# Kernel optimization log

Hardware: AMD Instinct MI355X
Metric: run time of the kernel (lower is better)

## Reference

```python
import jax, jax.numpy as jnp
import numpy as np

NUM_HEADS = 8
H_DIM = 24
COORDS_DIM = 3
NUM_W_PER_DIST = 8
BLOCK_SIZE = 128
N_HASHES = 3
N = 32768
HASH_DIM = H_DIM + (COORDS_DIM - 1) + 2  # q/k augmented with RPE coordinate terms


def layernorm(x, g, b, eps=1e-5):
    mu = x.mean(-1, keepdims=True)
    var = ((x - mu) ** 2).mean(-1, keepdims=True)
    return (x - mu) * jax.lax.rsqrt(var + eps) * g + b


def setup_inputs() -> dict:
    key = jax.random.key(0)
    ks = jax.random.split(key, 16)
    d, H = H_DIM, NUM_HEADS
    s = lambda i, shape, scale: jax.random.normal(ks[i], shape, jnp.float32) * scale
    return {
        "x": s(0, (N, d), 1.0),
        "coords": jax.random.uniform(ks[1], (N, COORDS_DIM), jnp.float32),
        "norm1_g": jnp.ones((d,), jnp.float32),
        "norm1_b": jnp.zeros((d,), jnp.float32),
        "Wq": s(2, (d, H * d), d ** -0.5),
        "Wk": s(3, (d, H * d), d ** -0.5),
        "Wv": s(4, (d, H * d), d ** -0.5),
        "w_rpe_W": s(5, (H * d, (COORDS_DIM - 1) * NUM_W_PER_DIST), 0.3),
        "Wo": s(6, (H * d, d), (H * d) ** -0.5),
        "bo": jnp.zeros((d,), jnp.float32),
        "norm2_g": jnp.ones((d,), jnp.float32),
        "norm2_b": jnp.zeros((d,), jnp.float32),
        "ff_W1": s(7, (d, d), d ** -0.5),
        "ff_b1": jnp.zeros((d,), jnp.float32),
        "ff_W2": s(8, (d, d), d ** -0.5),
        "ff_b2": jnp.zeros((d,), jnp.float32),
        "alphas": s(9, (N_HASHES, H, HASH_DIM), 1.0),  # E2LSH projection vectors
    }


def hept_attention(q, k, v, coords, w_rpe_W, alphas):
    # q,k,v: [n, H*d]. HEPT: fold RPE exp(-w*||dp||^2) into augmented q/k, then
    # n_hashes rounds of LSH sort + block-local attention, combined by softmax
    # over each round's log-normalizer (Reformer-style).
    n = q.shape[0]
    H, d, B = NUM_HEADS, H_DIM, BLOCK_SIZE
    nb = n // B
    q = q.reshape(n, H, d).transpose(1, 0, 2) * (d ** -0.5)  # [H,n,d]
    k = k.reshape(n, H, d).transpose(1, 0, 2)
    v = v.reshape(n, H, d).transpose(1, 0, 2)
    # per-head non-negative distance weights from w_rpe (mixture collapsed)
    Wm = w_rpe_W.reshape(H, d, COORDS_DIM - 1, NUM_W_PER_DIST)
    w = jnp.mean(Wm, axis=(1, 3)) ** 2                        # [H, c-1]
    p = coords[:, 1:]                                          # [n, c-1]
    sqn = jnp.einsum("hc,nc,nc->hn", w, p, p)                # w*||p||^2
    qp = jnp.sqrt(2.0) * jnp.sqrt(w)[:, None, :] * p[None]     # [H,n,c-1]
    ones = jnp.ones((H, n, 1), q.dtype)
    # q_hat.k_hat = q.k + 2*w*p_i.p_j - w|p_i|^2 - w|p_j|^2 = q.k - w*||p_i-p_j||^2
    q_hat = jnp.concatenate([q, qp, -sqn[..., None], ones], -1)  # [H,n,HASH_DIM]
    k_hat = jnp.concatenate([k, qp, ones, -sqn[..., None]], -1)
    outs, zs = [], []
    for r in range(N_HASHES):
        a = alphas[r]                                          # [H, HASH_DIM]
        iq = jnp.argsort(jnp.einsum("hne,he->hn", q_hat, a), -1)
        ik = jnp.argsort(jnp.einsum("hne,he->hn", k_hat, a), -1)
        qs = jnp.take_along_axis(q_hat, iq[..., None], 1).reshape(H, nb, B, -1)
        ks = jnp.take_along_axis(k_hat, ik[..., None], 1).reshape(H, nb, B, -1)
        vs = jnp.take_along_axis(v, ik[..., None], 1).reshape(H, nb, B, d)
        logits = jnp.einsum("hbqe,hbke->hbqk", qs, ks)         # [H,nb,B,B]
        z = jax.nn.logsumexp(logits, -1).reshape(H, n)
        o = jnp.einsum("hbqk,hbkd->hbqd", jax.nn.softmax(logits, -1), vs).reshape(H, n, d)
        inv = jnp.argsort(iq, -1)                              # unsort to input order
        outs.append(jnp.take_along_axis(o, inv[..., None], 1))
        zs.append(jnp.take_along_axis(z, inv, 1))
    wts = jax.nn.softmax(jnp.stack(zs), axis=0)[..., None]     # [R,H,n,1]
    out = (jnp.stack(outs) * wts).sum(0)                       # [H,n,d]
    return out.transpose(1, 0, 2).reshape(n, H * d)


def reference(x, coords, norm1_g, norm1_b, Wq, Wk, Wv, w_rpe_W, Wo, bo,
              norm2_g, norm2_b, ff_W1, ff_b1, ff_W2, ff_b2, alphas):
    xn = layernorm(x, norm1_g, norm1_b)
    q, k, v = xn @ Wq, xn @ Wk, xn @ Wv
    aggr = hept_attention(q, k, v, coords, w_rpe_W, alphas) @ Wo + bo
    x = x + aggr  # dropout is identity in eval mode
    h = layernorm(x, norm2_g, norm2_b)
    ff = jax.nn.relu(h @ ff_W1 + ff_b1) @ ff_W2 + ff_b2
    return x + ff
```

## Files before the change

kernel.cpp:

```cpp
#include <hip/hip_runtime.h>
#include <math.h>

#define NPT 32768
#define NH 8
#define HD 24
#define EDIM 28
#define NHASH 3
#define NSEG 48
#define NRH 24

typedef unsigned long long u64;
typedef unsigned short ushort;
typedef __attribute__((__vector_size__(8 * sizeof(short)))) short bf16x8;
typedef __attribute__((__vector_size__(4 * sizeof(float)))) float floatx4;
typedef __attribute__((__vector_size__(4 * sizeof(unsigned int)))) unsigned int uint32x4;

__device__ __forceinline__ ushort f2bf(float f) {
    unsigned u = __float_as_uint(f);
    unsigned r = u + 0x7FFF + ((u >> 16) & 1);
    return (ushort)(r >> 16);
}
__device__ __forceinline__ float us2f(ushort u) {
    return __uint_as_float(((unsigned)u) << 16);
}

__global__ __launch_bounds__(256) void k0b(
    const float* __restrict__ wrpe, const float* __restrict__ Wq,
    const float* __restrict__ Wk, const float* __restrict__ alphas,
    double* __restrict__ w64, double* __restrict__ cqp64,
    double* __restrict__ Aq, double* __restrict__ Ak, double* __restrict__ ct) {
    __shared__ double sw[16], sc[16];
    int t = threadIdx.x;
    if (t < 16) {
        int h = t >> 1, c = t & 1;
        double s = 0.0;
        for (int i = 0; i < 24; i++)
            for (int j = 0; j < 8; j++)
                s += (double)wrpe[(h * 24 + i) * 16 + c * 8 + j];
        double m = s / 192.0;
        sw[t] = m * m;
        sc[t] = sqrt(2.0) * fabs(m);
        w64[t] = sw[t];
        cqp64[t] = sc[t];
    }
    __syncthreads();
    const double QSCALE = 1.0 / sqrt(24.0);
    for (int idx = t; idx < 24 * NRH; idx += 256) {
        int i = idx / NRH, rh = idx % NRH;
        int h = rh & 7;
        double aq = 0.0, ak = 0.0;
        for (int e = 0; e < 24; e++) {
            double al = (double)alphas[rh * 28 + e];
            aq += (double)Wq[i * 192 + h * 24 + e] * al;
            ak += (double)Wk[i * 192 + h * 24 + e] * al;
        }
        Aq[idx] = aq * QSCALE;
        Ak[idx] = ak;
    }
    if (t < NRH) {
        int h = t & 7;
        ct[t * 4 + 0] = (double)alphas[t * 28 + 24] * sc[h * 2 + 0];
        ct[t * 4 + 1] = (double)alphas[t * 28 + 25] * sc[h * 2 + 1];
        ct[t * 4 + 2] = (double)alphas[t * 28 + 26];
        ct[t * 4 + 3] = (double)alphas[t * 28 + 27];
    }
}

__global__ __launch_bounds__(512) void k2s(
    const float* __restrict__ x, const float* __restrict__ n1g,
    const float* __restrict__ n1b, const float* __restrict__ coords,
    const double* __restrict__ Aq, const double* __restrict__ Ak,
    const double* __restrict__ ct, const double* __restrict__ w64,
    u64* __restrict__ keys, float* __restrict__ xnf) {
    __shared__ double sA[2][24][NRH];
    __shared__ double sCt[NRH][4];
    __shared__ double sW64[16];
    __shared__ double sGB[48];
    __shared__ double sXn[8][24];
    int t = threadIdx.x;
    for (int i = t; i < 24 * NRH; i += 512) sA[0][i / NRH][i % NRH] = Aq[i];
    for (int i = t; i < 24 * NRH; i += 512) sA[1][i / NRH][i % NRH] = Ak[i];
    for (int i = t; i < NRH * 4; i += 512) sCt[i / 4][i % 4] = ct[i];
    if (t < 16) sW64[t] = w64[t];
    if (t < 24) { sGB[t] = (double)n1g[t]; sGB[24 + t] = (double)n1b[t]; }
    __syncthreads();
    int wv = t >> 6, l = t & 63;
    for (int g = 0; g < 8; g++) {
        int n = blockIdx.x * 64 + g * 8 + wv;
        double xv = (l < 24) ? (double)x[(u64)n * 24 + l] : 0.0;
        double s = xv;
        s += __shfl_xor(s, 1); s += __shfl_xor(s, 2); s += __shfl_xor(s, 4);
        s += __shfl_xor(s, 8); s += __shfl_xor(s, 16);
        double mu = s / 24.0;
        double d = (l < 24) ? (xv - mu) : 0.0;
        double v2 = d * d;
        v2 += __shfl_xor(v2, 1); v2 += __shfl_xor(v2, 2); v2 += __shfl_xor(v2, 4);
        v2 += __shfl_xor(v2, 8); v2 += __shfl_xor(v2, 16);
        double rstd = 1.0 / sqrt(v2 / 24.0 + 1e-5);
        if (l < 24) {
            double xn = d * rstd * sGB[l] + sGB[24 + l];
            sXn[wv][l] = xn;
            xnf[(u64)n * 24 + l] = (float)xn;
        }
        double p0 = (double)coords[(u64)n * 3 + 1];
        double p1 = (double)coords[(u64)n * 3 + 2];
        if (l < 2 * NRH) {
            int qk = l / NRH, rh = l % NRH;
            int h = rh & 7;
            double sqn = sW64[2 * h] * p0 * p0 + sW64[2 * h + 1] * p1 * p1;
            double acc = sCt[rh][0] * p0 + sCt[rh][1] * p1;
            acc += qk ? (sCt[rh][2] - sqn * sCt[rh][3]) : (sCt[rh][3] - sqn * sCt[rh][2]);
            for (int i = 0; i < 24; i++) acc += sXn[wv][i] * sA[qk][i][rh];
            u64 u = (u64)__double_as_longlong(acc);
            if (u >> 63) u = ~u; else u |= 0x8000000000000000ULL;
            u64 key = (u & ~(u64)32767) | (u64)n;
            keys[(u64)l * NPT + n] = key;
        }
    }
}

#define K2P_PTS 32
__global__ __launch_bounds__(640) void k2p(
    const float* __restrict__ xnf,
    const float* __restrict__ Wq, const float* __restrict__ Wk,
    const float* __restrict__ Wv, const float* __restrict__ coords,
    const double* __restrict__ w64, const double* __restrict__ cqp64,
    ushort* __restrict__ qhatB, ushort* __restrict__ khatB, ushort* __restrict__ varrB) {
    __shared__ __align__(16) ushort sT[3 * 8 * K2P_PTS * 32];
    int t = threadIdx.x;
    int n0 = blockIdx.x * K2P_PTS;
    if (t < 576) {
        int m = t / 192, jj = t % 192;
        const float* W = (m == 0) ? Wq : ((m == 1) ? Wk : Wv);
        float wc[24];
#pragma unroll
        for (int i = 0; i < 24; i++) wc[i] = W[i * 192 + jj];
        const float scale = (m == 0) ? (float)(1.0 / sqrt(24.0)) : 1.0f;
        int h = jj / 24, e = jj % 24;
        ushort* sbase = sT + ((m * 8 + h) * K2P_PTS) * 32 + e;
        for (int p = 0; p < K2P_PTS; p++) {
            int n = n0 + p;
            const float* xr = xnf + (u64)n * 24;
            float acc = 0.f;
#pragma unroll
            for (int i = 0; i < 24; i++) acc += xr[i] * wc[i];
            sbase[p * 32] = f2bf(acc * scale);
        }
    } else {
        int l = t - 576;
        int h2 = l >> 3, e2 = 24 + (l & 7);
        double c0 = cqp64[h2 * 2], c1 = cqp64[h2 * 2 + 1];
        double wa = w64[h2 * 2], wb = w64[h2 * 2 + 1];
        ushort* qb = sT + ((0 * 8 + h2) * K2P_PTS) * 32 + e2;
        ushort* kb = sT + ((1 * 8 + h2) * K2P_PTS) * 32 + e2;
        ushort* vb = sT + ((2 * 8 + h2) * K2P_PTS) * 32 + e2;
        for (int p = 0; p < K2P_PTS; p++) {
            int n = n0 + p;
            double p0 = (double)coords[(u64)n * 3 + 1];
            double p1 = (double)coords[(u64)n * 3 + 2];
            float qv, kv;
            if (e2 < 26) {
                int c = e2 - 24;
                float qp = (float)((c ? c1 : c0) * (c ? p1 : p0));
                qv = qp; kv = qp;
            } else if (e2 < 28) {
                double sqn = wa * p0 * p0 + wb * p1 * p1;
                if (e2 == 26) { qv = (float)(-sqn); kv = 1.0f; }
                else          { qv = 1.0f; kv = (float)(-sqn); }
            } else {
                qv = 0.0f; kv = 0.0f;
            }
            qb[p * 32] = f2bf(qv);
            kb[p * 32] = f2bf(kv);
            vb[p * 32] = 0;
        }
    }
    __syncthreads();
    for (int c = t; c < 3 * 8 * K2P_PTS * 4; c += 640) {
        int arrh = c >> 7, off = c & 127;
        int arr = arrh >> 3, hh = arrh & 7;
        uint32x4 v = *(const uint32x4*)(sT + arrh * (K2P_PTS * 32) + off * 8);
        ushort* op = (arr == 0) ? qhatB : ((arr == 1) ? khatB : varrB);
        *(uint32x4*)(op + (u64)hh * NPT * 32 + (u64)n0 * 32 + off * 8) = v;
    }
}

__device__ __forceinline__ u64 shflx64(u64 v, int d) {
    int lo = __shfl_xor((int)(unsigned)v, d);
    int hi = __shfl_xor((int)(unsigned)(v >> 32), d);
    return ((u64)(unsigned)hi << 32) | (unsigned)lo;
}
__device__ __forceinline__ void cswap(u64& a, u64& b, bool up) {
    if ((a > b) == up) { u64 tmp = a; a = b; b = tmp; }
}
__device__ __forceinline__ u64* sslot(u64* s, int i) {
    int a = i << 3;
    a ^= ((a >> 9) & 7) << 4;
    return (u64*)((char*)s + a);
}
__device__ __forceinline__ void reg_passes(u64 e[8], int ib, int K, int jmax) {
    for (int j = jmax; j >= 1; j >>= 1) {
#pragma unroll
        for (int k = 0; k < 8; k++)
            if ((k & j) == 0) cswap(e[k], e[k | j], ((ib + k) & K) == 0);
    }
}
__device__ __forceinline__ void shfl_passes(u64 e[8], int t, int segoff, int K, int jhi, int jlo) {
    for (int j = jhi; j >= jlo; j >>= 1) {
        int d = j >> 3;
        bool lower = (t & d) == 0;
        bool up = ((segoff + ((t & ~d) << 3)) & K) == 0;
        bool keepmin = (lower == up);
#pragma unroll
        for (int k = 0; k < 8; k++) {
            u64 o = shflx64(e[k], d);
            bool ownsm = e[k] < o;
            e[k] = (ownsm == keepmin) ? e[k] : o;
        }
    }
}

__global__ __launch_bounds__(1024) void sort_local_full(u64* keys) {
    __shared__ u64 s[8192];
    int t = threadIdx.x;
    u64 gbase = (u64)blockIdx.x * 8192;
    int segoff = (int)(gbase & 32767);
    int ib = segoff + t * 8;
    u64 e[8];
#pragma unroll
    for (int k = 0; k < 8; k++) e[k] = keys[gbase + t * 8 + k];
    reg_passes(e, ib, 2, 1);
    reg_passes(e, ib, 4, 2);
    reg_passes(e, ib, 8, 4);
    for (int K = 16; K <= 512; K <<= 1) {
        shfl_passes(e, t, segoff, K, K >> 1, 8);
        reg_passes(e, ib, K, 4);
    }
#pragma unroll
    for (int k = 0; k < 8; k++) *sslot(s, t * 8 + k) = e[k];
    __syncthreads();
    for (int K = 1024; K <= 8192; K <<= 1) {
        for (int j = K >> 1; j >= 512; j >>= 1) {
            for (int p = t; p < 4096; p += 1024) {
                int i = ((p & ~(j - 1)) << 1) | (p & (j - 1));
                int i2 = i | j;
                bool up = (((segoff + i) & K) == 0);
                u64 a = *sslot(s, i), b = *sslot(s, i2);
                if ((a > b) == up) { *sslot(s, i) = b; *sslot(s, i2) = a; }
            }
            __syncthreads();
        }
#pragma unroll
        for (int k = 0; k < 8; k++) e[k] = *sslot(s, t * 8 + k);
        shfl_passes(e, t, segoff, K, 256, 8);
        reg_passes(e, ib, K, 4);
        if (K < 8192) {
#pragma unroll
            for (int k = 0; k < 8; k++) *sslot(s, t * 8 + k) = e[k];
            __syncthreads();
        } else {
#pragma unroll
            for (int k = 0; k < 8; k++) keys[gbase + t * 8 + k] = e[k];
        }
    }
}

__global__ __launch_bounds__(1024) void sort_tail1_fused(u64* keys) {
    __shared__ u64 s[8192];
    int t = threadIdx.x;
    u64 gbase = (u64)blockIdx.x * 8192;
    u64 pbase = gbase ^ 8192ULL;
    int ci = (int)((gbase >> 13) & 3);
    bool keepmin = (ci == 0) || (ci == 3);
    int segoff = (int)(gbase & 32767);
    int ib = segoff + t * 8;
    for (int i = t; i < 8192; i += 1024) {
        u64 a = keys[gbase + i];
        u64 b = keys[pbase + i];
        u64 mn = a < b ? a : b;
        u64 mx = a < b ? b : a;
        *sslot(s, i) = keepmin ? mn : mx;
    }
    __syncthreads();
    const int K = 16384;
    for (int j = 4096; j >= 512; j >>= 1) {
        for (int p = t; p < 4096; p += 1024) {
            int i = ((p & ~(j - 1)) << 1) | (p & (j - 1));
            int i2 = i | j;
            bool up = (((segoff + i) & K) == 0);
            u64 a = *sslot(s, i), b = *sslot(s, i2);
            if ((a > b) == up) { *sslot(s, i) = b; *sslot(s, i2) = a; }
        }
        __syncthreads();
    }
    u64 e[8];
#pragma unroll
    for (int k = 0; k < 8; k++) e[k] = *sslot(s, t * 8 + k);
    shfl_passes(e, t, segoff, K, 256, 8);
    reg_passes(e, ib, K, 4);
#pragma unroll
    for (int k = 0; k < 8; k++) keys[gbase + t * 8 + k] = e[k];
}

__global__ __launch_bounds__(1024) void sort_local_tail(u64* keys, int K, int minj) {
    __shared__ u64 s[8192];
    int t = threadIdx.x;
    u64 gbase = (u64)blockIdx.x * 8192;
    int segoff = (int)(gbase & 32767);
    int ib = segoff + t * 8;
    for (int i = t; i < 8192; i += 1024) *sslot(s, i) = keys[gbase + i];
    __syncthreads();
    for (int j = 4096; j >= 512; j >>= 1) {
        for (int p = t; p < 4096; p += 1024) {
            int i = ((p & ~(j - 1)) << 1) | (p & (j - 1));
            int i2 = i | j;
            bool up = (((segoff + i) & K) == 0);
            u64 a = *sslot(s, i), b = *sslot(s, i2);
            if ((a > b) == up) { *sslot(s, i) = b; *sslot(s, i2) = a; }
        }
        __syncthreads();
    }
    u64 e[8];
#pragma unroll
    for (int k = 0; k < 8; k++) e[k] = *sslot(s, t * 8 + k);
    shfl_passes(e, t, segoff, K, 256, minj >= 8 ? minj : 8);
    if (minj < 8) reg_passes(e, ib, K, 4);
#pragma unroll
    for (int k = 0; k < 8; k++) keys[gbase + t * 8 + k] = e[k];
}

__global__ void sort_global2(u64* keys) {
    int p = blockIdx.x * blockDim.x + threadIdx.x;
    if (p >= NSEG * 8192) return;
    int seg = p >> 13, c = p & 8191;
    u64 base = (u64)seg * 32768 + c;
    u64 e0 = keys[base];
    u64 e1 = keys[base + 8192];
    u64 e2 = keys[base + 16384];
    u64 e3 = keys[base + 24576];
    u64 tmp;
    if (e0 > e2) { tmp = e0; e0 = e2; e2 = tmp; }
    if (e1 > e3) { tmp = e1; e1 = e3; e3 = tmp; }
    if (e0 > e1) { tmp = e0; e0 = e1; e1 = tmp; }
    if (e2 > e3) { tmp = e2; e2 = e3; e3 = tmp; }
    keys[base] = e0;
    keys[base + 8192] = e1;
    keys[base + 16384] = e2;
    keys[base + 24576] = e3;
}

__global__ __launch_bounds__(256, 4) void k3_attn(
    const u64* __restrict__ keys, const ushort* __restrict__ qhatB,
    const ushort* __restrict__ khatB, const ushort* __restrict__ varrB,
    ushort* __restrict__ ozB) {
    int rh3 = blockIdx.x % 24;
    int b = blockIdx.x / 24;
    int h = rh3 & 7, r = rh3 >> 3;
    __shared__ __align__(16) char smem[6144 + 32768 + 512];
    char* sVt = smem;
    char* sP  = smem + 6144;
    ushort* qidx = (ushort*)(smem + 6144 + 32768);
    ushort* kidx = qidx + 128;
    int t = threadIdx.x;
    int segQ = r * 8 + h, segK = 24 + r * 8 + h;
    if (t < 128) {
        qidx[t] = (ushort)(keys[(u64)segQ * NPT + b * 128 + t] & 32767ULL);
    } else {
        int i = t - 128;
        kidx[i] = (ushort)(keys[(u64)segK * NPT + b * 128 + i] & 32767ULL);
    }
    __syncthreads();

    int wave = t >> 6, L = t & 63;
    int quad = L >> 4, n16 = L & 15;

    const bf16x8* Qg = (const bf16x8*)(qhatB + (u64)h * NPT * 32);
    const bf16x8* Kg = (const bf16x8*)(khatB + (u64)h * NPT * 32);
    bf16x8 afr[2];
#pragma unroll
    for (int rtg = 0; rtg < 2; rtg++) {
        int qi = qidx[wave * 32 + rtg * 16 + n16];
        afr[rtg] = Qg[(u64)qi * 4 + quad];
    }
    bf16x8 bfr[8];
#pragma unroll
    for (int ct = 0; ct < 8; ct++) {
        int ki = kidx[ct * 16 + n16];
        bfr[ct] = Kg[(u64)ki * 4 + quad];
    }
    if (t < 128) {
        int ki = kidx[t];
        const bf16x8* vr = (const bf16x8*)(varrB + ((u64)h * NPT + ki) * 32);
        bf16x8 v0 = vr[0], v1 = vr[1], v2 = vr[2];
        int colb = ((t & 15) << 4) | ((t >> 4) << 1);
#pragma unroll
        for (int e = 0; e < 8; e++) {
            int e0 = e, e1 = 8 + e, e2 = 16 + e;
            *(short*)(sVt + e0 * 256 + (colb ^ ((e0 & 7) << 4))) = v0[e];
            *(short*)(sVt + e1 * 256 + (colb ^ ((e1 & 7) << 4))) = v1[e];
            *(short*)(sVt + e2 * 256 + (colb ^ ((e2 & 7) << 4))) = v2[e];
        }
    }
    __syncthreads();

    floatx4 acc[2][8];
#pragma unroll
    for (int rtg = 0; rtg < 2; rtg++)
#pragma unroll
        for (int ct = 0; ct < 8; ct++)
            acc[rtg][ct] = (floatx4){0.f, 0.f, 0.f, 0.f};
#pragma unroll
    for (int ct = 0; ct < 8; ct++) {
#pragma unroll
        for (int rtg = 0; rtg < 2; rtg++)
            acc[rtg][ct] = __builtin_amdgcn_mfma_f32_16x16x32_bf16(afr[rtg], bfr[ct], acc[rtg][ct], 0, 0, 0);
    }

    float mrow[2][4], srow[2][4];
#pragma unroll
    for (int rtg = 0; rtg < 2; rtg++) {
#pragma unroll
        for (int rg = 0; rg < 4; rg++) {
            float m = acc[rtg][0][rg];
#pragma unroll
            for (int ct = 1; ct < 8; ct++) m = fmaxf(m, acc[rtg][ct][rg]);
            m = fmaxf(m, __shfl_xor(m, 1));
            m = fmaxf(m, __shfl_xor(m, 2));
            m = fmaxf(m, __shfl_xor(m, 4));
            m = fmaxf(m, __shfl_xor(m, 8));
            mrow[rtg][rg] = m;
            float p[8];
            float s = 0.0f;
#pragma unroll
            for (int ct = 0; ct < 8; ct++) {
                p[ct] = __expf(acc[rtg][ct][rg] - m);
                s += p[ct];
            }
            s += __shfl_xor(s, 1);
            s += __shfl_xor(s, 2);
            s += __shfl_xor(s, 4);
            s += __shfl_xor(s, 8);
            srow[rtg][rg] = s;
            unsigned w0, w1, w2, w3;
            asm("v_cvt_pk_bf16_f32 %0, %1, %2" : "=v"(w0) : "v"(p[0]), "v"(p[1]));
            asm("v_cvt_pk_bf16_f32 %0, %1, %2" : "=v"(w1) : "v"(p[2]), "v"(p[3]));
            asm("v_cvt_pk_bf16_f32 %0, %1, %2" : "=v"(w2) : "v"(p[4]), "v"(p[5]));
            asm("v_cvt_pk_bf16_f32 %0, %1, %2" : "=v"(w3) : "v"(p[6]), "v"(p[7]));
            int row = wave * 32 + rtg * 16 + quad * 4 + rg;
            uint32x4 pk = {w0, w1, w2, w3};
            *(uint32x4*)(sP + row * 256 + (((n16 << 4)) ^ ((row & 7) << 4))) = pk;
        }
    }

    floatx4 occ[2][2];
#pragma unroll
    for (int rtg = 0; rtg < 2; rtg++)
#pragma unroll
        for (int ct2 = 0; ct2 < 2; ct2++)
            occ[rtg][ct2] = (floatx4){0.f, 0.f, 0.f, 0.f};
#pragma unroll
    for (int ks = 0; ks < 4; ks++) {
        int kb = ks * 64 + quad * 16;
        bf16x8 bv[2], av[2];
#pragma unroll
        for (int ct2 = 0; ct2 < 2; ct2++) {
            int e = ct2 * 16 + n16;
            int ec = (e < 24) ? e : 0;
            bv[ct2] = *(const bf16x8*)(sVt + ec * 256 + (kb ^ ((ec & 7) << 4)));
        }
#pragma unroll
        for (int rtg = 0; rtg < 2; rtg++) {
            int rowA = wave * 32 + rtg * 16 + n16;
            av[rtg] = *(const bf16x8*)(sP + rowA * 256 + (kb ^ ((rowA & 7) << 4)));
        }
#pragma unroll
        for (int rtg = 0; rtg < 2; rtg++)
#pragma unroll
            for (int ct2 = 0; ct2 < 2; ct2++)
                occ[rtg][ct2] = __builtin_amdgcn_mfma_f32_16x16x32_bf16(av[rtg], bv[ct2], occ[rtg][ct2], 0, 0, 0);
    }

#pragma unroll
    for (int rtg = 0; rtg < 2; rtg++) {
#pragma unroll
        for (int rg = 0; rg < 4; rg++) {
            int row = wave * 32 + rtg * 16 + quad * 4 + rg;
            int oi = qidx[row];
            float inv = 1.0f / srow[rtg][rg];
            ushort* orow = ozB + ((u64)segQ * NPT + oi) * 32;
#pragma unroll
            for (int ct2 = 0; ct2 < 2; ct2++) {
                int col = ct2 * 16 + n16;
                if (col < 24) orow[col] = f2bf(occ[rtg][ct2][rg] * inv);
            }
            if (n16 == 0)
                *(float*)(orow + 24) = mrow[rtg][rg] + __logf(srow[rtg][rg]);
        }
    }
}

#define K4PTS 32
#define AT_STR 196
#define W_STR 28
__global__ __launch_bounds__(256) void k4_final(
    const ushort* __restrict__ ozB,
    const float* __restrict__ x,
    const float* __restrict__ Wo, const float* __restrict__ bo,
    const float* __restrict__ g2, const float* __restrict__ b2,
    const float* __restrict__ W1, const float* __restrict__ b1f,
    const float* __restrict__ W2, const float* __restrict__ b2f,
    float* __restrict__ out) {
    __shared__ __align__(16) float sWoT[24][AT_STR];
    __shared__ __align__(16) float sW1T[24][W_STR], sW2T[24][W_STR];
    __shared__ float sB[5 * 24];
    __shared__ __align__(16) float attn[K4PTS][AT_STR];
    __shared__ float xrow[K4PTS][25];
    __shared__ __align__(16) float h2row[K4PTS][W_STR];
    __shared__ __align__(16) float ffrow[K4PTS][W_STR];
    int t = threadIdx.x;
    int base = blockIdx.x * K4PTS;
    for (int i = t; i < 4608; i += 256) sWoT[i % 24][i / 24] = Wo[i];
    for (int i = t; i < 576; i += 256) {
        sW1T[i % 24][i / 24] = W1[i];
        sW2T[i % 24][i / 24] = W2[i];
    }
    if (t < 24) {
        sB[t] = bo[t]; sB[24 + t] = g2[t]; sB[48 + t] = b2[t];
        sB[72 + t] = b1f[t]; sB[96 + t] = b2f[t];
    }
    if (t < K4PTS * 4) {
        int p = t >> 2, c = 24 + (t & 3);
        h2row[p][c] = 0.f; ffrow[p][c] = 0.f;
    }
    if (t < 24 * 4) {
        int rr = t >> 2, c = 24 + (t & 3);
        sW1T[rr][c] = 0.f; sW2T[rr][c] = 0.f;
    }
    {
        int p = t >> 3, h = t & 7;
        int n = base + p;
        const ushort* r0 = ozB + ((u64)(0 * 8 + h) * NPT + n) * 32;
        const ushort* r1 = ozB + ((u64)(1 * 8 + h) * NPT + n) * 32;
        const ushort* r2 = ozB + ((u64)(2 * 8 + h) * NPT + n) * 32;
        float z0 = *(const float*)(r0 + 24);
        float z1 = *(const float*)(r1 + 24);
        float z2 = *(const float*)(r2 + 24);
        float zm = fmaxf(z0, fmaxf(z1, z2));
        float e0 = __expf(z0 - zm), e1 = __expf(z1 - zm), e2 = __expf(z2 - zm);
        float inv = 1.0f / (e0 + e1 + e2);
        float w0 = e0 * inv, w1 = e1 * inv, w2 = e2 * inv;
#pragma unroll
        for (int e = 0; e < 24; e++)
            attn[p][h * 24 + e] = w0 * us2f(r0[e]) + w1 * us2f(r1[e]) + w2 * us2f(r2[e]);
    }
    __syncthreads();
    int p = t >> 3, oe = t & 7;
    int n = base + p;
    {
        const floatx4* ap = (const floatx4*)&attn[p][0];
        const floatx4* w0p = (const floatx4*)&sWoT[oe][0];
        const floatx4* w1p = (const floatx4*)&sWoT[oe + 8][0];
        const floatx4* w2p = (const floatx4*)&sWoT[oe + 16][0];
        floatx4 A0 = {0.f, 0.f, 0.f, 0.f}, A1 = A0, A2 = A0;
        for (int ii = 0; ii < 48; ii++) {
            floatx4 av = ap[ii];
            A0 += av * w0p[ii];
            A1 += av * w1p[ii];
            A2 += av * w2p[ii];
        }
        float a0 = A0[0] + A0[1] + A0[2] + A0[3];
        float a1 = A1[0] + A1[1] + A1[2] + A1[3];
        float a2 = A2[0] + A2[1] + A2[2] + A2[3];
        xrow[p][oe]      = x[n * 24 + oe]      + a0 + sB[oe];
        xrow[p][oe + 8]  = x[n * 24 + oe + 8]  + a1 + sB[oe + 8];
        xrow[p][oe + 16] = x[n * 24 + oe + 16] + a2 + sB[oe + 16];
    }
    float mu, rstd;
    {
        float s = xrow[p][oe] + xrow[p][oe + 8] + xrow[p][oe + 16];
        s += __shfl_xor(s, 1); s += __shfl_xor(s, 2); s += __shfl_xor(s, 4);
        mu = s / 24.0f;
        float v0 = xrow[p][oe] - mu, v1 = xrow[p][oe + 8] - mu, v2 = xrow[p][oe + 16] - mu;
        float v = v0 * v0 + v1 * v1 + v2 * v2;
        v += __shfl_xor(v, 1); v += __shfl_xor(v, 2); v += __shfl_xor(v, 4);
        rstd = 1.0f / sqrtf(v / 24.0f + 1e-5f);
    }
    h2row[p][oe]      = (xrow[p][oe] - mu)      * rstd * sB[24 + oe]      + sB[48 + oe];
    h2row[p][oe + 8]  = (xrow[p][oe + 8] - mu)  * rstd * sB[24 + oe + 8]  + sB[48 + oe + 8];
    h2row[p][oe + 16] = (xrow[p][oe + 16] - mu) * rstd * sB[24 + oe + 16] + sB[48 + oe + 16];
    {
        const floatx4* hp = (const floatx4*)&h2row[p][0];
        const floatx4* w0p = (const floatx4*)&sW1T[oe][0];
        const floatx4* w1p = (const floatx4*)&sW1T[oe + 8][0];
        const floatx4* w2p = (const floatx4*)&sW1T[oe + 16][0];
        floatx4 A0 = {0.f, 0.f, 0.f, 0.f}, A1 = A0, A2 = A0;
#pragma unroll
        for (int ii = 0; ii < 6; ii++) {
            floatx4 hv = hp[ii];
            A0 += hv * w0p[ii];
            A1 += hv * w1p[ii];
            A2 += hv * w2p[ii];
        }
        ffrow[p][oe]      = fmaxf(A0[0]+A0[1]+A0[2]+A0[3] + sB[72 + oe], 0.f);
        ffrow[p][oe + 8]  = fmaxf(A1[0]+A1[1]+A1[2]+A1[3] + sB[72 + oe + 8], 0.f);
        ffrow[p][oe + 16] = fmaxf(A2[0]+A2[1]+A2[2]+A2[3] + sB[72 + oe + 16], 0.f);
    }
    {
        const floatx4* fp = (const floatx4*)&ffrow[p][0];
        const floatx4* w0p = (const floatx4*)&sW2T[oe][0];
        const floatx4* w1p = (const floatx4*)&sW2T[oe + 8][0];
        const floatx4* w2p = (const floatx4*)&sW2T[oe + 16][0];
        floatx4 A0 = {0.f, 0.f, 0.f, 0.f}, A1 = A0, A2 = A0;
#pragma unroll
        for (int ii = 0; ii < 6; ii++) {
            floatx4 fv = fp[ii];
            A0 += fv * w0p[ii];
            A1 += fv * w1p[ii];
            A2 += fv * w2p[ii];
        }
        out[n * 24 + oe]      = xrow[p][oe]      + A0[0]+A0[1]+A0[2]+A0[3] + sB[96 + oe];
        out[n * 24 + oe + 8]  = xrow[p][oe + 8]  + A1[0]+A1[1]+A1[2]+A1[3] + sB[96 + oe + 8];
        out[n * 24 + oe + 16] = xrow[p][oe + 16] + A2[0]+A2[1]+A2[2]+A2[3] + sB[96 + oe + 16];
    }
}

extern "C" void kernel_launch(void* const* d_in, const int* in_sizes, int n_in,
                              void* d_out, int out_size, void* d_ws, size_t ws_size,
                              hipStream_t stream) {
    const float* x      = (const float*)d_in[0];
    const float* coords = (const float*)d_in[1];
    const float* n1g    = (const float*)d_in[2];
    const float* n1b    = (const float*)d_in[3];
    const float* Wq     = (const float*)d_in[4];
    const float* Wk     = (const float*)d_in[5];
    const float* Wv     = (const float*)d_in[6];
    const float* wrpe   = (const float*)d_in[7];
    const float* Wo     = (const float*)d_in[8];
    const float* bo     = (const float*)d_in[9];
    const float* n2g    = (const float*)d_in[10];
    const float* n2b    = (const float*)d_in[11];
    const float* W1     = (const float*)d_in[12];
    const float* b1     = (const float*)d_in[13];
    const float* W2     = (const float*)d_in[14];
    const float* b2     = (const float*)d_in[15];
    const float* alphas = (const float*)d_in[16];

    char* ws = (char*)d_ws;
    size_t off = 0;
    auto alloc = [&](size_t bytes) -> void* {
        void* p = ws + off;
        off = (off + bytes + 255) & ~(size_t)255;
        return p;
    };
    double* w64   = (double*)alloc(256);
    double* cqp   = (double*)alloc(256);
    double* Aq    = (double*)alloc(24 * NRH * 8);
    double* Ak    = (double*)alloc(24 * NRH * 8);
    double* ct    = (double*)alloc(NRH * 4 * 8);
    float*  xnf   = (float*)alloc((size_t)NPT * 24 * 4);
    ushort* qhatB = (ushort*)alloc((size_t)NH * NPT * 32 * 2);
    ushort* khatB = (ushort*)alloc((size_t)NH * NPT * 32 * 2);
    ushort* varrB = (ushort*)alloc((size_t)NH * NPT * 32 * 2);
    u64*    keys  = (u64*)alloc((size_t)NSEG * NPT * 8);
    ushort* ozB   = (ushort*)alloc((size_t)NHASH * NH * NPT * 32 * 2);
    if (off > ws_size) return;

    k0b<<<1, 256, 0, stream>>>(wrpe, Wq, Wk, alphas, w64, cqp, Aq, Ak, ct);
    k2s<<<NPT / 64, 512, 0, stream>>>(x, n1g, n1b, coords, Aq, Ak, ct, w64, keys, xnf);
    k2p<<<NPT / K2P_PTS, 640, 0, stream>>>(xnf, Wq, Wk, Wv, coords, w64, cqp,
                                           qhatB, khatB, varrB);
    sort_local_full<<<192, 1024, 0, stream>>>(keys);
    sort_tail1_fused<<<192, 1024, 0, stream>>>(keys);
    sort_global2<<<NSEG * 8192 / 256, 256, 0, stream>>>(keys);
    sort_local_tail<<<192, 1024, 0, stream>>>(keys, 32768, 128);
    k3_attn<<<256 * 8 * 3, 256, 0, stream>>>(keys, qhatB, khatB, varrB, ozB);
    k4_final<<<NPT / K4PTS, 256, 0, stream>>>(ozB, x, Wo, bo, n2g, n2b,
                                              W1, b1, W2, b2, (float*)d_out);
}
```

Baseline: 305.6 us.

## Stage K through LDS in attention, fold log2e into Q, add MFMA priority

K rows for each block are now loaded once, cooperatively by half the threads, and staged in LDS, instead of every wave gathering all 128 K rows from global memory. V staging moves to the other half of the threads. Q is prescaled by 1/ln2 so the softmax can use exp2f, and the log-normalizer is converted back with ln2. MFMA sections get s_setprio hints. The larger LDS footprint lowers the occupancy hint from 4 to 3 blocks, which may reduce latency hiding, and the bf16 rounding of the prescaled Q changes slightly.

```diff
diff --git a/kernel.cpp b/kernel.cpp
--- a/kernel.cpp
+++ b/kernel.cpp
@@ -120,6 +120,7 @@
 }
 
 #define K2P_PTS 32
+#define INVLN2F 1.4426950408889634f
 __global__ __launch_bounds__(640) void k2p(
     const float* __restrict__ xnf,
     const float* __restrict__ Wq, const float* __restrict__ Wk,
@@ -135,7 +136,7 @@
         float wc[24];
 #pragma unroll
         for (int i = 0; i < 24; i++) wc[i] = W[i * 192 + jj];
-        const float scale = (m == 0) ? (float)(1.0 / sqrt(24.0)) : 1.0f;
+        const float scale = (m == 0) ? (float)(1.4426950408889634 / sqrt(24.0)) : 1.0f;
         int h = jj / 24, e = jj % 24;
         ushort* sbase = sT + ((m * 8 + h) * K2P_PTS) * 32 + e;
         for (int p = 0; p < K2P_PTS; p++) {
@@ -170,7 +171,7 @@
             } else {
                 qv = 0.0f; kv = 0.0f;
             }
-            qb[p * 32] = f2bf(qv);
+            qb[p * 32] = f2bf(qv * INVLN2F);
             kb[p * 32] = f2bf(kv);
             vb[p * 32] = 0;
         }
@@ -349,17 +350,18 @@
     keys[base + 24576] = e3;
 }
 
-__global__ __launch_bounds__(256, 4) void k3_attn(
+__global__ __launch_bounds__(256, 3) void k3_attn(
     const u64* __restrict__ keys, const ushort* __restrict__ qhatB,
     const ushort* __restrict__ khatB, const ushort* __restrict__ varrB,
     ushort* __restrict__ ozB) {
     int rh3 = blockIdx.x % 24;
     int b = blockIdx.x / 24;
     int h = rh3 & 7, r = rh3 >> 3;
-    __shared__ __align__(16) char smem[6144 + 32768 + 512];
-    char* sVt = smem;
-    char* sP  = smem + 6144;
-    ushort* qidx = (ushort*)(smem + 6144 + 32768);
+    __shared__ __align__(16) char smem[9216 + 6144 + 32768 + 512];
+    char* sK  = smem;
+    char* sVt = smem + 9216;
+    char* sP  = smem + 15360;
+    ushort* qidx = (ushort*)(smem + 48128);
     ushort* kidx = qidx + 128;
     int t = threadIdx.x;
     int segQ = r * 8 + h, segK = 24 + r * 8 + h;
@@ -375,24 +377,27 @@
     int quad = L >> 4, n16 = L & 15;
 
     const bf16x8* Qg = (const bf16x8*)(qhatB + (u64)h * NPT * 32);
-    const bf16x8* Kg = (const bf16x8*)(khatB + (u64)h * NPT * 32);
     bf16x8 afr[2];
 #pragma unroll
     for (int rtg = 0; rtg < 2; rtg++) {
         int qi = qidx[wave * 32 + rtg * 16 + n16];
         afr[rtg] = Qg[(u64)qi * 4 + quad];
     }
-    bf16x8 bfr[8];
-#pragma unroll
-    for (int ct = 0; ct < 8; ct++) {
-        int ki = kidx[ct * 16 + n16];
-        bfr[ct] = Kg[(u64)ki * 4 + quad];
-    }
     if (t < 128) {
         int ki = kidx[t];
+        const uint32x4* kr = (const uint32x4*)(khatB + ((u64)h * NPT + ki) * 32);
+        uint32x4 a0 = kr[0], a1 = kr[1], a2 = kr[2], a3 = kr[3];
+        char* dst = sK + t * 72;
+        *(uint32x4*)(dst)      = a0;
+        *(uint32x4*)(dst + 16) = a1;
+        *(uint32x4*)(dst + 32) = a2;
+        *(uint32x4*)(dst + 48) = a3;
+    } else {
+        int tv = t - 128;
+        int ki = kidx[tv];
         const bf16x8* vr = (const bf16x8*)(varrB + ((u64)h * NPT + ki) * 32);
         bf16x8 v0 = vr[0], v1 = vr[1], v2 = vr[2];
-        int colb = ((t & 15) << 4) | ((t >> 4) << 1);
+        int colb = ((tv & 15) << 4) | ((tv >> 4) << 1);
 #pragma unroll
         for (int e = 0; e < 8; e++) {
             int e0 = e, e1 = 8 + e, e2 = 16 + e;
@@ -403,18 +408,25 @@
     }
     __syncthreads();
 
+    bf16x8 bfr[8];
+#pragma unroll
+    for (int ct = 0; ct < 8; ct++)
+        bfr[ct] = *(const bf16x8*)(sK + (ct * 16 + n16) * 72 + quad * 16);
+
     floatx4 acc[2][8];
 #pragma unroll
     for (int rtg = 0; rtg < 2; rtg++)
 #pragma unroll
         for (int ct = 0; ct < 8; ct++)
             acc[rtg][ct] = (floatx4){0.f, 0.f, 0.f, 0.f};
+    __builtin_amdgcn_s_setprio(1);
 #pragma unroll
     for (int ct = 0; ct < 8; ct++) {
 #pragma unroll
         for (int rtg = 0; rtg < 2; rtg++)
             acc[rtg][ct] = __builtin_amdgcn_mfma_f32_16x16x32_bf16(afr[rtg], bfr[ct], acc[rtg][ct], 0, 0, 0);
     }
+    __builtin_amdgcn_s_setprio(0);
 
     float mrow[2][4], srow[2][4];
 #pragma unroll
@@ -433,7 +445,7 @@
             float s = 0.0f;
 #pragma unroll
             for (int ct = 0; ct < 8; ct++) {
-                p[ct] = __expf(acc[rtg][ct][rg] - m);
+                p[ct] = exp2f(acc[rtg][ct][rg] - m);
                 s += p[ct];
             }
             s += __shfl_xor(s, 1);
@@ -473,13 +485,16 @@
             int rowA = wave * 32 + rtg * 16 + n16;
             av[rtg] = *(const bf16x8*)(sP + rowA * 256 + (kb ^ ((rowA & 7) << 4)));
         }
+        __builtin_amdgcn_s_setprio(1);
 #pragma unroll
         for (int rtg = 0; rtg < 2; rtg++)
 #pragma unroll
             for (int ct2 = 0; ct2 < 2; ct2++)
                 occ[rtg][ct2] = __builtin_amdgcn_mfma_f32_16x16x32_bf16(av[rtg], bv[ct2], occ[rtg][ct2], 0, 0, 0);
-    }
-
+        __builtin_amdgcn_s_setprio(0);
+    }
+
+    const float LN2F = 0.6931471805599453f;
 #pragma unroll
     for (int rtg = 0; rtg < 2; rtg++) {
 #pragma unroll
@@ -494,7 +509,7 @@
                 if (col < 24) orow[col] = f2bf(occ[rtg][ct2][rg] * inv);
             }
             if (n16 == 0)
-                *(float*)(orow + 24) = mrow[rtg][rg] + __logf(srow[rtg][rg]);
+                *(float*)(orow + 24) = mrow[rtg][rg] * LN2F + __logf(srow[rtg][rg]);
         }
     }
 }
```

Measured after the change: 333.6 us. +9.2%, slower.
